# Kernel tuning notes

Hardware: AMD Instinct MI355X
Metric: run time of the kernel (lower is better)

## Reference

```python
import jax, jax.numpy as jnp
import numpy as np

B, NS, H = 131072, 64, 32
# e3nn path normalization (irrep_normalization='component', path_normalization='element')
PW1_0 = float((NS * NS + 25.0) ** -0.5)            # paths into hidden 0e: sqrt(1/(NS^2 + 5*5))
PW1_2 = float((5.0 / (10.0 * NS + 25.0)) ** 0.5)   # paths into hidden 2e: sqrt(5/(NS*5 + 5*NS + 25))
PW2_2 = float((5.0 / (3.0 * H * H)) ** 0.5)        # paths into output 2e: sqrt(5/(3*H^2))
INV_S5 = float(5.0 ** -0.5)                        # w3j(0,2,2) = delta/sqrt(5); w3j(2,2,0) = delta/sqrt(5)

def _wigner3j_222():
    # Real l=2 basis as orthonormal symmetric traceless 3x3 matrices (tr(Ma Mb)=delta).
    # C_abc = tr(sym(Ma Mb) Mc), fully symmetric invariant 3-tensor, Frobenius-normalized to 1
    # (the real Wigner 3j for (2,2,2), up to basis orientation convention).
    s2, s6 = np.sqrt(2.0), np.sqrt(6.0)
    M = np.zeros((5, 3, 3))
    M[0] = np.array([[0., 1, 0], [1, 0, 0], [0, 0, 0]]) / s2   # xy
    M[1] = np.array([[0., 0, 0], [0, 0, 1], [0, 1, 0]]) / s2   # yz
    M[2] = np.diag([-1., -1, 2]) / s6                           # 2z^2-x^2-y^2
    M[3] = np.array([[0., 0, 1], [0, 0, 0], [1, 0, 0]]) / s2   # xz
    M[4] = np.diag([1., -1, 0]) / s2                            # x^2-y^2
    C = np.einsum('aij,bjk,cki->abc', M, M, M)
    C = 0.5 * (C + C.transpose(1, 0, 2))
    return C / np.linalg.norm(C)

C222 = jnp.asarray(_wigner3j_222(), dtype=jnp.float32)

def setup_inputs() -> dict:
    key = jax.random.key(0)
    ks = jax.random.split(key, 14)
    f = jnp.float32
    return {
        'scalars': jax.random.normal(ks[0], (B, NS), f),
        'kernel_t2_sum': jax.random.normal(ks[1], (B, 5), f),
        'mc_t2': jax.random.normal(ks[2], (B, 5), f),
        'coulomb_t2': jax.random.normal(ks[3], (B, 5), f),
        'bs_t2': jax.random.normal(ks[4], (B, 5), f),
        'mopac_coulomb_t2': jax.random.normal(ks[5], (B, 5), f),
        # tp1 weights (e3nn internal weights ~ N(0,1)), one (mul1,mul2,mul_out) block per path
        'w1_sss': jax.random.normal(ks[6], (NS, NS, H), f),   # 0e x 0e -> 0e
        'w1_stt': jax.random.normal(ks[7], (NS, 5, H), f),    # 0e x 2e -> 2e
        'w1_tst': jax.random.normal(ks[8], (5, NS, H), f),    # 2e x 0e -> 2e
        'w1_tts': jax.random.normal(ks[9], (5, 5, H), f),     # 2e x 2e -> 0e
        'w1_ttt': jax.random.normal(ks[10], (5, 5, H), f),    # 2e x 2e -> 2e
        # tp2 weights
        'w2_stt': jax.random.normal(ks[11], (H, H, 1), f),
        'w2_tst': jax.random.normal(ks[12], (H, H, 1), f),
        'w2_ttt': jax.random.normal(ks[13], (H, H, 1), f),
    }

def _forward(scalars, kernel_t2_sum, mc_t2, coulomb_t2, bs_t2, mopac_coulomb_t2,
             w1_sss, w1_stt, w1_tst, w1_tts, w1_ttt, w2_stt, w2_tst, w2_ttt):
    s = scalars                                                        # (B, NS) : NS x 0e
    t = jnp.stack([kernel_t2_sum, mc_t2, coulomb_t2, bs_t2,
                   mopac_coulomb_t2], axis=1)
    # tp1: x (x) x -> hidden (H x 0e + H x 2e)
    h_s = PW1_0 * (jnp.einsum('uvw,bu,bv->bw', w1_sss, s, s)
                   + INV_S5 * jnp.einsum('uvw,bui,bvi->bw', w1_tts, t, t))          # (B, H)
    h_t = PW1_2 * (INV_S5 * jnp.einsum('uvw,bu,bvk->bwk', w1_stt, s, t)
                   + INV_S5 * jnp.einsum('uvw,buk,bv->bwk', w1_tst, t, s)
                   + jnp.einsum('uvw,ijk,bui,bvj->bwk', w1_ttt, C222, t, t))        # (B, H, 5)
    out = PW2_2 * (INV_S5 * jnp.einsum('uvw,bu,bvk->bwk', w2_stt, h_s, h_t)
                   + INV_S5 * jnp.einsum('uvw,buk,bv->bwk', w2_tst, h_t, h_s)
                   + jnp.einsum('uvw,ijk,bui,bvj->bwk', w2_ttt, C222, h_t, h_t))    # (B, 1, 5)
    return out[:, 0, :]                                                             # (B, 5)

def reference(scalars, kernel_t2_sum, mc_t2, coulomb_t2, bs_t2, mopac_coulomb_t2,
              w1_sss, w1_stt, w1_tst, w1_tts, w1_ttt, w2_stt, w2_tst, w2_ttt):
    return _forward(scalars, kernel_t2_sum, mc_t2, coulomb_t2, bs_t2, mopac_coulomb_t2,
                    w1_sss, w1_stt, w1_tst, w1_tts, w1_ttt, w2_stt, w2_tst, w2_ttt)
```

## Files before the change

### kernel.cpp

```cpp
#include <hip/hip_runtime.h>
#include <math.h>
#include <stdint.h>


#define CW1 0.23904572186687872f
#define CW2 0.20701966780270626f
#define CW3 0.11952286093343936f

typedef float f32x4 __attribute__((ext_vector_type(4)));
typedef short bf16x8 __attribute__((ext_vector_type(8)));
typedef uint32_t u32x4 __attribute__((ext_vector_type(4)));

__device__ __forceinline__ uint32_t f2bf(float f) {
  uint32_t x = __float_as_uint(f);
  return (x + 0x7fffu + ((x >> 16) & 1u)) >> 16;
}
__device__ __forceinline__ uint32_t packbf(float lo, float hi) {
  return f2bf(lo) | (f2bf(hi) << 16);
}
__device__ __forceinline__ float bflo(uint32_t d) { return __uint_as_float(d << 16); }
__device__ __forceinline__ float bfhi(uint32_t d) { return __uint_as_float(d & 0xffff0000u); }

#define MF16(a, b, c) __builtin_amdgcn_mfma_f32_16x16x32_bf16((a), (b), (c), 0, 0, 0)

__device__ __align__(16) uint32_t g_bsss16[64 * 2 * 2 * 64 * 4];
__device__ __align__(16) uint32_t g_bst16[5 * 2 * 2 * 64 * 4];
__device__ __align__(16) uint32_t g_btts16[2 * 64 * 4];
__device__ __align__(16) uint32_t g_bttt16[2 * 64 * 4];
__device__ __align__(16) uint32_t g_bg2_16[2 * 64 * 4];
__device__ __align__(16) uint32_t g_bgt16[2 * 64 * 4];

__device__ const int c_pu[16] = {0,0,0,0,0,1,1,1,1,2,2,2,3,3,4,0};
__device__ const int c_pv[16] = {0,1,2,3,4,1,2,3,4,2,3,4,3,4,4,0};

__global__ void ech_prep(const float* __restrict__ w1_sss, const float* __restrict__ w1_stt,
                         const float* __restrict__ w1_tst, const float* __restrict__ w1_tts,
                         const float* __restrict__ w1_ttt, const float* __restrict__ w2_stt,
                         const float* __restrict__ w2_tst, const float* __restrict__ w2_ttt) {
  const float PW1_0 = (float)(1.0 / sqrt(4121.0));
  const float PW1_2 = (float)sqrt(5.0 / 665.0);
  const float PW2_2 = (float)sqrt(5.0 / 3072.0);
  const float IS5   = (float)sqrt(0.2);

  int idx = blockIdx.x * 256 + threadIdx.x;

  if (idx < 65536) {
    int d = idx & 3, l = (idx >> 2) & 63, c = (idx >> 8) & 1, n = (idx >> 9) & 1, v = idx >> 10;
    int gg = l >> 4, w = n * 16 + (l & 15);
    int u0 = 32 * c + 8 * gg + 2 * d, u1 = u0 + 1;
    float lo = 0.f, hi = 0.f;
    if (u0 < v)       lo = w1_sss[(u0 * 64 + v) * 32 + w] + w1_sss[(v * 64 + u0) * 32 + w];
    else if (u0 == v) lo = w1_sss[(u0 * 64 + v) * 32 + w];
    if (u1 < v)       hi = w1_sss[(u1 * 64 + v) * 32 + w] + w1_sss[(v * 64 + u1) * 32 + w];
    else if (u1 == v) hi = w1_sss[(u1 * 64 + v) * 32 + w];
    g_bsss16[idx] = packbf(PW1_0 * lo, PW1_0 * hi);
    return;
  }
  idx -= 65536;
  if (idx < 5120) {
    int d = idx & 3, l = (idx >> 2) & 63, c = (idx >> 8) & 1, n = (idx >> 9) & 1, ct = idx >> 10;
    int gg = l >> 4, w = n * 16 + (l & 15);
    float sc = PW1_2 * IS5;
    int u0 = 32 * c + 8 * gg + 2 * d, u1 = u0 + 1;
    g_bst16[idx] = packbf(sc * (w1_stt[(u0 * 5 + ct) * 32 + w] + w1_tst[(ct * 64 + u0) * 32 + w]),
                          sc * (w1_stt[(u1 * 5 + ct) * 32 + w] + w1_tst[(ct * 64 + u1) * 32 + w]));
    return;
  }
  idx -= 5120;
  if (idx < 512) {
    int d = idx & 3, l = (idx >> 2) & 63, n = idx >> 8;
    int gg = l >> 4, w = n * 16 + (l & 15);
    float sc = PW1_0 * IS5;
    float val[2];
#pragma unroll
    for (int q = 0; q < 2; ++q) {
      int p = 8 * gg + 2 * d + q;
      float x = 0.f;
      if (p < 15) {
        int u = c_pu[p], v = c_pv[p];
        x = w1_tts[(u * 5 + v) * 32 + w];
        if (u < v) x += w1_tts[(v * 5 + u) * 32 + w];
        x *= sc;
      }
      val[q] = x;
    }
    g_btts16[idx] = packbf(val[0], val[1]);
    return;
  }
  idx -= 512;
  if (idx < 512) {
    int d = idx & 3, l = (idx >> 2) & 63, n = idx >> 8;
    int gg = l >> 4, w = n * 16 + (l & 15);
    float val[2];
#pragma unroll
    for (int q = 0; q < 2; ++q) {
      int p = 8 * gg + 2 * d + q;
      float x = 0.f;
      if (p < 15) {
        int u = c_pu[p], v = c_pv[p];
        x = w1_ttt[(u * 5 + v) * 32 + w];
        if (u < v) x += w1_ttt[(v * 5 + u) * 32 + w];
        x *= PW1_2;
      }
      val[q] = x;
    }
    g_bttt16[idx] = packbf(val[0], val[1]);
    return;
  }
  idx -= 512;
  if (idx < 512) {
    int d = idx & 3, l = (idx >> 2) & 63, n = idx >> 8;
    int gg = l >> 4, v = n * 16 + (l & 15);
    float sc = PW2_2 * IS5;
    int u0 = 8 * gg + 2 * d, u1 = u0 + 1;
    g_bg2_16[idx] = packbf(sc * (w2_stt[u0 * 32 + v] + w2_tst[v * 32 + u0]),
                           sc * (w2_stt[u1 * 32 + v] + w2_tst[v * 32 + u1]));
    return;
  }
  idx -= 512;
  if (idx < 512) {
    int d = idx & 3, l = (idx >> 2) & 63, n = idx >> 8;
    int gg = l >> 4, v = n * 16 + (l & 15);
    int u0 = 8 * gg + 2 * d, u1 = u0 + 1;
    g_bgt16[idx] = packbf(PW2_2 * w2_ttt[u0 * 32 + v], PW2_2 * w2_ttt[u1 * 32 + v]);
    return;
  }
}

#define S_STRIDE 33
#define OFF_SF 2112
#define SF_STRIDE 65
#define OFF_T 6272
#define ED_STRIDE 49
#define PLANE(i) ((i) * 1088)
#define LDS_DW 7872

__global__ __launch_bounds__(256, 2)
void ech_fused(const float* __restrict__ scalars,
               const float* __restrict__ tk, const float* __restrict__ tm,
               const float* __restrict__ tc, const float* __restrict__ tb,
               const float* __restrict__ tmc,
               float* __restrict__ out) {
  __shared__ uint32_t lds[LDS_DW];

  const int tid = threadIdx.x;
  const int rows64 = blockIdx.x * 64;
  const int wave = tid >> 6, lane = tid & 63;
  const int g = lane >> 4, col16 = lane & 15;
  const int wrow = wave * 16;
  const f32x4 zero4 = {0.f, 0.f, 0.f, 0.f};

#pragma unroll
  for (int it = 0; it < 8; ++it) {
    int di = it * 256 + tid;
    int row = di >> 5, j = di & 31;
    float f0 = scalars[(rows64 + row) * 64 + 2 * j];
    float f1 = scalars[(rows64 + row) * 64 + 2 * j + 1];
    lds[row * S_STRIDE + j] = packbf(f0, f1);
    lds[OFF_SF + row * SF_STRIDE + 2 * j]     = __float_as_uint(f0);
    lds[OFF_SF + row * SF_STRIDE + 2 * j + 1] = __float_as_uint(f1);
  }
#pragma unroll
  for (int v = 0; v < 5; ++v) {
    const float* p = (v == 0 ? tk : v == 1 ? tm : v == 2 ? tc : v == 3 ? tb : tmc);
#pragma unroll
    for (int it = 0; it < 2; ++it) {
      int i = it * 256 + tid;
      if (i < 320)
        lds[OFF_T + (i / 5) * 25 + v * 5 + (i % 5)] = __float_as_uint(p[rows64 * 5 + i]);
    }
  }
  __syncthreads();

  bf16x8 afr_hi[2];
#pragma unroll
  for (int c = 0; c < 2; ++c) {
    int base = (wrow + col16) * S_STRIDE + 16 * c + 4 * g;
    u32x4 th;
    th.x = lds[base + 0]; th.y = lds[base + 1];
    th.z = lds[base + 2]; th.w = lds[base + 3];
    afr_hi[c] = __builtin_bit_cast(bf16x8, th);
  }

  f32x4 hsA = zero4, hsB = zero4;
  const bf16x8* gb = (const bf16x8*)g_bsss16;
#pragma unroll 2
  for (int vd = 0; vd < 16; ++vd) {
    int v0 = 2 * vd, v1 = v0 + 1;
    bf16x8 b00 = gb[(v0 * 4 + 0) * 64 + lane];
    bf16x8 b01 = gb[(v0 * 4 + 2) * 64 + lane];
    bf16x8 b10 = gb[(v1 * 4 + 0) * 64 + lane];
    bf16x8 b11 = gb[(v1 * 4 + 2) * 64 + lane];
    f32x4 Z00 = MF16(afr_hi[0], b00, zero4);
    f32x4 Z01 = MF16(afr_hi[0], b01, zero4);
    f32x4 Z10 = MF16(afr_hi[0], b10, zero4);
    f32x4 Z11 = MF16(afr_hi[0], b11, zero4);
#pragma unroll
    for (int r = 0; r < 4; ++r) {
      int row = wrow + 4 * g + r;
      float s0 = __uint_as_float(lds[OFF_SF + row * SF_STRIDE + v0]);
      float s1 = __uint_as_float(lds[OFF_SF + row * SF_STRIDE + v1]);
      hsA[r] = fmaf(s0, Z00[r], hsA[r]); hsA[r] = fmaf(s1, Z10[r], hsA[r]);
      hsB[r] = fmaf(s0, Z01[r], hsB[r]); hsB[r] = fmaf(s1, Z11[r], hsB[r]);
    }
  }
#pragma unroll 2
  for (int vd = 16; vd < 32; ++vd) {
    int v0 = 2 * vd, v1 = v0 + 1;
    f32x4 Z00 = zero4, Z01 = zero4, Z10 = zero4, Z11 = zero4;
#pragma unroll
    for (int c = 0; c < 2; ++c) {
      bf16x8 b00 = gb[(v0 * 4 + 0 + c) * 64 + lane];
      bf16x8 b01 = gb[(v0 * 4 + 2 + c) * 64 + lane];
      bf16x8 b10 = gb[(v1 * 4 + 0 + c) * 64 + lane];
      bf16x8 b11 = gb[(v1 * 4 + 2 + c) * 64 + lane];
      Z00 = MF16(afr_hi[c], b00, Z00);
      Z01 = MF16(afr_hi[c], b01, Z01);
      Z10 = MF16(afr_hi[c], b10, Z10);
      Z11 = MF16(afr_hi[c], b11, Z11);
    }
#pragma unroll
    for (int r = 0; r < 4; ++r) {
      int row = wrow + 4 * g + r;
      float s0 = __uint_as_float(lds[OFF_SF + row * SF_STRIDE + v0]);
      float s1 = __uint_as_float(lds[OFF_SF + row * SF_STRIDE + v1]);
      hsA[r] = fmaf(s0, Z00[r], hsA[r]); hsA[r] = fmaf(s1, Z10[r], hsA[r]);
      hsB[r] = fmaf(s0, Z01[r], hsB[r]); hsB[r] = fmaf(s1, Z11[r], hsB[r]);
    }
  }

  f32x4 ht[5][2];
#pragma unroll
  for (int k = 0; k < 5; ++k) { ht[k][0] = zero4; ht[k][1] = zero4; }
  {
    const bf16x8* gs = (const bf16x8*)g_bst16;
#pragma unroll
    for (int ct = 0; ct < 5; ++ct) {
      f32x4 a0 = zero4, a1 = zero4;
#pragma unroll
      for (int c = 0; c < 2; ++c) {
        bf16x8 b0 = gs[(ct * 4 + 0 + c) * 64 + lane];
        bf16x8 b1 = gs[(ct * 4 + 2 + c) * 64 + lane];
        a0 = MF16(afr_hi[c], b0, a0);
        a1 = MF16(afr_hi[c], b1, a1);
      }
#pragma unroll
      for (int r = 0; r < 4; ++r) {
        int row = wrow + 4 * g + r;
        int tbi = OFF_T + row * 25 + ct * 5;
        float t0 = __uint_as_float(lds[tbi + 0]);
        float t1 = __uint_as_float(lds[tbi + 1]);
        float t2 = __uint_as_float(lds[tbi + 2]);
        float t3 = __uint_as_float(lds[tbi + 3]);
        float t4 = __uint_as_float(lds[tbi + 4]);
        ht[0][0][r] = fmaf(a0[r], t0, ht[0][0][r]); ht[0][1][r] = fmaf(a1[r], t0, ht[0][1][r]);
        ht[1][0][r] = fmaf(a0[r], t1, ht[1][0][r]); ht[1][1][r] = fmaf(a1[r], t1, ht[1][1][r]);
        ht[2][0][r] = fmaf(a0[r], t2, ht[2][0][r]); ht[2][1][r] = fmaf(a1[r], t2, ht[2][1][r]);
        ht[3][0][r] = fmaf(a0[r], t3, ht[3][0][r]); ht[3][1][r] = fmaf(a1[r], t3, ht[3][1][r]);
        ht[4][0][r] = fmaf(a0[r], t4, ht[4][0][r]); ht[4][1][r] = fmaf(a1[r], t4, ht[4][1][r]);
      }
    }
  }
  __syncthreads();

  {
    int row = tid >> 2, part = tid & 3;
    int tbase = OFF_T + row * 25;
    float P[4][6];
#pragma unroll
    for (int q = 0; q < 4; ++q) {
      int p = part * 4 + q;
      int U = c_pu[p], V = c_pv[p];
      float a0 = __uint_as_float(lds[tbase + U * 5 + 0]);
      float a1 = __uint_as_float(lds[tbase + U * 5 + 1]);
      float a2 = __uint_as_float(lds[tbase + U * 5 + 2]);
      float a3 = __uint_as_float(lds[tbase + U * 5 + 3]);
      float a4 = __uint_as_float(lds[tbase + U * 5 + 4]);
      float b0 = __uint_as_float(lds[tbase + V * 5 + 0]);
      float b1 = __uint_as_float(lds[tbase + V * 5 + 1]);
      float b2 = __uint_as_float(lds[tbase + V * 5 + 2]);
      float b3 = __uint_as_float(lds[tbase + V * 5 + 3]);
      float b4 = __uint_as_float(lds[tbase + V * 5 + 4]);
      float d0 = a0 * b0, d1 = a1 * b1, d2 = a2 * b2, d3 = a3 * b3, d4 = a4 * b4;
      float s01 = a0 * b1 + a1 * b0;
      float s02 = a0 * b2 + a2 * b0;
      float s03 = a0 * b3 + a3 * b0;
      float s12 = a1 * b2 + a2 * b1;
      float s13 = a1 * b3 + a3 * b1;
      float s14 = a1 * b4 + a4 * b1;
      float s23 = a2 * b3 + a3 * b2;
      float s24 = a2 * b4 + a4 * b2;
      float s34 = a3 * b4 + a4 * b3;
      P[q][0] = -CW1 * s02 + CW2 * s13;
      P[q][1] = CW2 * s03 + CW3 * s12 - CW2 * s14;
      P[q][2] = -CW1 * d0 + CW3 * d1 + CW1 * d2 + CW3 * d3 - CW1 * d4;
      P[q][3] = CW2 * s01 + CW3 * s23 + CW2 * s34;
      P[q][4] = -CW2 * d1 - CW1 * s24 + CW2 * d3;
      P[q][5] = d0 + d1 + d2 + d3 + d4;
      if (p == 15) {
#pragma unroll
        for (int c6 = 0; c6 < 6; ++c6) P[q][c6] = 0.f;
      }
    }
    int rb = row * ED_STRIDE + part * 2;
#pragma unroll
    for (int comp = 0; comp < 6; ++comp) {
      lds[rb + comp * 8 + 0] = packbf(P[0][comp], P[1][comp]);
      lds[rb + comp * 8 + 1] = packbf(P[2][comp], P[3][comp]);
    }
  }
  __syncthreads();

  {
    int arow = wrow + col16;
    int gl = g & 1;
    bool gok = (g < 2);
    {
      int b5 = arow * ED_STRIDE + 40 + 4 * gl;
      u32x4 tmp;
      tmp.x = gok ? lds[b5 + 0] : 0u;
      tmp.y = gok ? lds[b5 + 1] : 0u;
      tmp.z = gok ? lds[b5 + 2] : 0u;
      tmp.w = gok ? lds[b5 + 3] : 0u;
      bf16x8 dfr = __builtin_bit_cast(bf16x8, tmp);
      hsA = MF16(dfr, ((const bf16x8*)g_btts16)[lane], hsA);
      hsB = MF16(dfr, ((const bf16x8*)g_btts16)[64 + lane], hsB);
    }
    bf16x8 btt0 = ((const bf16x8*)g_bttt16)[lane];
    bf16x8 btt1 = ((const bf16x8*)g_bttt16)[64 + lane];
#pragma unroll
    for (int k = 0; k < 5; ++k) {
      int bk = arow * ED_STRIDE + k * 8 + 4 * gl;
      u32x4 tmp;
      tmp.x = gok ? lds[bk + 0] : 0u;
      tmp.y = gok ? lds[bk + 1] : 0u;
      tmp.z = gok ? lds[bk + 2] : 0u;
      tmp.w = gok ? lds[bk + 3] : 0u;
      bf16x8 efr = __builtin_bit_cast(bf16x8, tmp);
      ht[k][0] = MF16(efr, btt0, ht[k][0]);
      ht[k][1] = MF16(efr, btt1, ht[k][1]);
    }
  }
  __syncthreads();

#pragma unroll
  for (int r = 0; r < 4; ++r) {
    int row = wrow + 4 * g + r;
    int dwb = row * 17 + (col16 >> 1);
    float pA = __shfl_xor(hsA[r], 1, 64);
    float pB = __shfl_xor(hsB[r], 1, 64);
    if (!(col16 & 1)) {
      lds[PLANE(0) + dwb]     = packbf(hsA[r], pA);
      lds[PLANE(0) + dwb + 8] = packbf(hsB[r], pB);
    }
#pragma unroll
    for (int k = 0; k < 5; ++k) {
      float qA = __shfl_xor(ht[k][0][r], 1, 64);
      float qB = __shfl_xor(ht[k][1][r], 1, 64);
      if (!(col16 & 1)) {
        lds[PLANE(1 + k) + dwb]     = packbf(ht[k][0][r], qA);
        lds[PLANE(1 + k) + dwb + 8] = packbf(ht[k][1][r], qB);
      }
    }
  }

  f32x4 g2n[2];
  {
    int prow = wrow + col16;
    int b = PLANE(0) + prow * 17 + 4 * g;
    u32x4 tmp;
    tmp.x = lds[b]; tmp.y = lds[b + 1]; tmp.z = lds[b + 2]; tmp.w = lds[b + 3];
    bf16x8 af = __builtin_bit_cast(bf16x8, tmp);
    g2n[0] = MF16(af, ((const bf16x8*)g_bg2_16)[lane], zero4);
    g2n[1] = MF16(af, ((const bf16x8*)g_bg2_16)[64 + lane], zero4);
  }
  f32x4 gt[5][2];
#pragma unroll
  for (int i = 0; i < 5; ++i) {
    int prow = wrow + col16;
    int b = PLANE(1 + i) + prow * 17 + 4 * g;
    u32x4 tmp;
    tmp.x = lds[b]; tmp.y = lds[b + 1]; tmp.z = lds[b + 2]; tmp.w = lds[b + 3];
    bf16x8 af = __builtin_bit_cast(bf16x8, tmp);
    gt[i][0] = MF16(af, ((const bf16x8*)g_bgt16)[lane], zero4);
    gt[i][1] = MF16(af, ((const bf16x8*)g_bgt16)[64 + lane], zero4);
  }

#define REDSTORE(K)                                                        \
  {                                                                        \
    _Pragma("unroll") for (int m = 1; m <= 8; m <<= 1)                     \
        _Pragma("unroll") for (int r = 0; r < 4; ++r)                      \
            tot[r] += __shfl_xor(tot[r], m, 64);                           \
    if (col16 == (K)) {                                                    \
      _Pragma("unroll") for (int r = 0; r < 4; ++r)                        \
          out[(size_t)(rows64 + wrow + 4 * g + r) * 5 + (K)] = tot[r];     \
    }                                                                      \
  }

  {
    float tot[4];
#pragma unroll
    for (int r = 0; r < 4; ++r) {
      float s = 0.f;
#pragma unroll
      for (int n = 0; n < 2; ++n) {
        float ok = g2n[n][r] * ht[0][n][r];
        ok = fmaf(-CW1, gt[0][n][r] * ht[2][n][r] + gt[2][n][r] * ht[0][n][r], ok);
        ok = fmaf( CW2, gt[1][n][r] * ht[3][n][r] + gt[3][n][r] * ht[1][n][r], ok);
        s += ok;
      }
      tot[r] = s;
    }
    REDSTORE(0)
  }
  {
    float tot[4];
#pragma unroll
    for (int r = 0; r < 4; ++r) {
      float s = 0.f;
#pragma unroll
      for (int n = 0; n < 2; ++n) {
        float ok = g2n[n][r] * ht[1][n][r];
        ok = fmaf( CW2, gt[0][n][r] * ht[3][n][r] + gt[3][n][r] * ht[0][n][r], ok);
        ok = fmaf( CW3, gt[1][n][r] * ht[2][n][r] + gt[2][n][r] * ht[1][n][r], ok);
        ok = fmaf(-CW2, gt[1][n][r] * ht[4][n][r] + gt[4][n][r] * ht[1][n][r], ok);
        s += ok;
      }
      tot[r] = s;
    }
    REDSTORE(1)
  }
  {
    float tot[4];
#pragma unroll
    for (int r = 0; r < 4; ++r) {
      float s = 0.f;
#pragma unroll
      for (int n = 0; n < 2; ++n) {
        float ok = g2n[n][r] * ht[2][n][r];
        ok = fmaf(-CW1, gt[0][n][r] * ht[0][n][r], ok);
        ok = fmaf( CW3, gt[1][n][r] * ht[1][n][r], ok);
        ok = fmaf( CW1, gt[2][n][r] * ht[2][n][r], ok);
        ok = fmaf( CW3, gt[3][n][r] * ht[3][n][r], ok);
        ok = fmaf(-CW1, gt[4][n][r] * ht[4][n][r], ok);
        s += ok;
      }
      tot[r] = s;
    }
    REDSTORE(2)
  }
  {
    float tot[4];
#pragma unroll
    for (int r = 0; r < 4; ++r) {
      float s = 0.f;
#pragma unroll
      for (int n = 0; n < 2; ++n) {
        float ok = g2n[n][r] * ht[3][n][r];
        ok = fmaf( CW2, gt[0][n][r] * ht[1][n][r] + gt[1][n][r] * ht[0][n][r], ok);
        ok = fmaf( CW3, gt[2][n][r] * ht[3][n][r] + gt[3][n][r] * ht[2][n][r], ok);
        ok = fmaf( CW2, gt[3][n][r] * ht[4][n][r] + gt[4][n][r] * ht[3][n][r], ok);
        s += ok;
      }
      tot[r] = s;
    }
    REDSTORE(3)
  }
  {
    float tot[4];
#pragma unroll
    for (int r = 0; r < 4; ++r) {
      float s = 0.f;
#pragma unroll
      for (int n = 0; n < 2; ++n) {
        float ok = g2n[n][r] * ht[4][n][r];
        ok = fmaf(-CW2, gt[1][n][r] * ht[1][n][r], ok);
        ok = fmaf(-CW1, gt[2][n][r] * ht[4][n][r] + gt[4][n][r] * ht[2][n][r], ok);
        ok = fmaf( CW2, gt[3][n][r] * ht[3][n][r], ok);
        s += ok;
      }
      tot[r] = s;
    }
    REDSTORE(4)
  }
}

extern "C" void kernel_launch(void* const* d_in, const int* in_sizes, int n_in,
                              void* d_out, int out_size, void* d_ws, size_t ws_size,
                              hipStream_t stream) {
  (void)n_in; (void)out_size; (void)d_ws; (void)ws_size;
  const float* scalars = (const float*)d_in[0];
  const float* tk  = (const float*)d_in[1];
  const float* tm  = (const float*)d_in[2];
  const float* tc  = (const float*)d_in[3];
  const float* tb  = (const float*)d_in[4];
  const float* tmc = (const float*)d_in[5];

  ech_prep<<<284, 256, 0, stream>>>((const float*)d_in[6], (const float*)d_in[7],
                                    (const float*)d_in[8], (const float*)d_in[9],
                                    (const float*)d_in[10], (const float*)d_in[11],
                                    (const float*)d_in[12], (const float*)d_in[13]);

  const int B = in_sizes[0] / 64;
  ech_fused<<<B / 64, 256, 0, stream>>>(scalars, tk, tm, tc, tb, tmc, (float*)d_out);
}
```

Measured before the change: 95.80 us.

## Split fused kernel into hidden-scalar kernel and remaining tensor-path kernel

Splits the single fused kernel into two launches. The first computes the scalar hidden features h_s with a smaller LDS footprint and higher launch-bounds occupancy, then writes them to a workspace buffer. The second re-reads scalars and the tensor inputs, loads h_s from the workspace, and does the rest. This aims to relieve register and LDS pressure in the heavy dense stage. The cost is an extra launch, a second read of scalars, and a round trip of the B×32 intermediate through global memory. Both branches of the workspace-size check run the same code, so an undersized workspace is not handled.

```diff
diff --git a/kernel.cpp b/kernel.cpp
--- a/kernel.cpp
+++ b/kernel.cpp
@@ -18,8 +18,6 @@
 __device__ __forceinline__ uint32_t packbf(float lo, float hi) {
   return f2bf(lo) | (f2bf(hi) << 16);
 }
-__device__ __forceinline__ float bflo(uint32_t d) { return __uint_as_float(d << 16); }
-__device__ __forceinline__ float bfhi(uint32_t d) { return __uint_as_float(d & 0xffff0000u); }
 
 #define MF16(a, b, c) __builtin_amdgcn_mfma_f32_16x16x32_bf16((a), (b), (c), 0, 0, 0)
 
@@ -127,22 +125,14 @@
   }
 }
 
-#define S_STRIDE 33
-#define OFF_SF 2112
-#define SF_STRIDE 65
-#define OFF_T 6272
-#define ED_STRIDE 49
-#define PLANE(i) ((i) * 1088)
-#define LDS_DW 7872
-
-__global__ __launch_bounds__(256, 2)
-void ech_fused(const float* __restrict__ scalars,
-               const float* __restrict__ tk, const float* __restrict__ tm,
-               const float* __restrict__ tc, const float* __restrict__ tb,
-               const float* __restrict__ tmc,
-               float* __restrict__ out) {
-  __shared__ uint32_t lds[LDS_DW];
-
+#define K1_SST 33
+#define K1_SF 2112
+#define K1_SFST 65
+#define K1_LDS 6272
+
+__global__ __launch_bounds__(256, 4)
+void ech_hs(const float* __restrict__ scalars, float* __restrict__ hsws) {
+  __shared__ uint32_t lds[K1_LDS];
   const int tid = threadIdx.x;
   const int rows64 = blockIdx.x * 64;
   const int wave = tid >> 6, lane = tid & 63;
@@ -156,26 +146,16 @@
     int row = di >> 5, j = di & 31;
     float f0 = scalars[(rows64 + row) * 64 + 2 * j];
     float f1 = scalars[(rows64 + row) * 64 + 2 * j + 1];
-    lds[row * S_STRIDE + j] = packbf(f0, f1);
-    lds[OFF_SF + row * SF_STRIDE + 2 * j]     = __float_as_uint(f0);
-    lds[OFF_SF + row * SF_STRIDE + 2 * j + 1] = __float_as_uint(f1);
-  }
-#pragma unroll
-  for (int v = 0; v < 5; ++v) {
-    const float* p = (v == 0 ? tk : v == 1 ? tm : v == 2 ? tc : v == 3 ? tb : tmc);
-#pragma unroll
-    for (int it = 0; it < 2; ++it) {
-      int i = it * 256 + tid;
-      if (i < 320)
-        lds[OFF_T + (i / 5) * 25 + v * 5 + (i % 5)] = __float_as_uint(p[rows64 * 5 + i]);
-    }
+    lds[row * K1_SST + j] = packbf(f0, f1);
+    lds[K1_SF + row * K1_SFST + 2 * j]     = __float_as_uint(f0);
+    lds[K1_SF + row * K1_SFST + 2 * j + 1] = __float_as_uint(f1);
   }
   __syncthreads();
 
   bf16x8 afr_hi[2];
 #pragma unroll
   for (int c = 0; c < 2; ++c) {
-    int base = (wrow + col16) * S_STRIDE + 16 * c + 4 * g;
+    int base = (wrow + col16) * K1_SST + 16 * c + 4 * g;
     u32x4 th;
     th.x = lds[base + 0]; th.y = lds[base + 1];
     th.z = lds[base + 2]; th.w = lds[base + 3];
@@ -198,8 +178,8 @@
 #pragma unroll
     for (int r = 0; r < 4; ++r) {
       int row = wrow + 4 * g + r;
-      float s0 = __uint_as_float(lds[OFF_SF + row * SF_STRIDE + v0]);
-      float s1 = __uint_as_float(lds[OFF_SF + row * SF_STRIDE + v1]);
+      float s0 = __uint_as_float(lds[K1_SF + row * K1_SFST + v0]);
+      float s1 = __uint_as_float(lds[K1_SF + row * K1_SFST + v1]);
       hsA[r] = fmaf(s0, Z00[r], hsA[r]); hsA[r] = fmaf(s1, Z10[r], hsA[r]);
       hsB[r] = fmaf(s0, Z01[r], hsB[r]); hsB[r] = fmaf(s1, Z11[r], hsB[r]);
     }
@@ -222,11 +202,79 @@
 #pragma unroll
     for (int r = 0; r < 4; ++r) {
       int row = wrow + 4 * g + r;
-      float s0 = __uint_as_float(lds[OFF_SF + row * SF_STRIDE + v0]);
-      float s1 = __uint_as_float(lds[OFF_SF + row * SF_STRIDE + v1]);
+      float s0 = __uint_as_float(lds[K1_SF + row * K1_SFST + v0]);
+      float s1 = __uint_as_float(lds[K1_SF + row * K1_SFST + v1]);
       hsA[r] = fmaf(s0, Z00[r], hsA[r]); hsA[r] = fmaf(s1, Z10[r], hsA[r]);
       hsB[r] = fmaf(s0, Z01[r], hsB[r]); hsB[r] = fmaf(s1, Z11[r], hsB[r]);
     }
+  }
+
+#pragma unroll
+  for (int r = 0; r < 4; ++r) {
+    size_t row = (size_t)(rows64 + wrow + 4 * g + r);
+    hsws[row * 32 + col16]      = hsA[r];
+    hsws[row * 32 + 16 + col16] = hsB[r];
+  }
+}
+
+#define K2_SST 33
+#define K2_T 2112
+#define K2_ED 3712
+#define ED_STRIDE 49
+#define PLANE(i) ((i) * 1088)
+#define K2_LDS 6848
+
+__global__ __launch_bounds__(256, 2)
+void ech_rest(const float* __restrict__ scalars,
+              const float* __restrict__ tk, const float* __restrict__ tm,
+              const float* __restrict__ tc, const float* __restrict__ tb,
+              const float* __restrict__ tmc,
+              const float* __restrict__ hsws,
+              float* __restrict__ out) {
+  __shared__ uint32_t lds[K2_LDS];
+  const int tid = threadIdx.x;
+  const int rows64 = blockIdx.x * 64;
+  const int wave = tid >> 6, lane = tid & 63;
+  const int g = lane >> 4, col16 = lane & 15;
+  const int wrow = wave * 16;
+  const f32x4 zero4 = {0.f, 0.f, 0.f, 0.f};
+
+#pragma unroll
+  for (int it = 0; it < 8; ++it) {
+    int di = it * 256 + tid;
+    int row = di >> 5, j = di & 31;
+    float f0 = scalars[(rows64 + row) * 64 + 2 * j];
+    float f1 = scalars[(rows64 + row) * 64 + 2 * j + 1];
+    lds[row * K2_SST + j] = packbf(f0, f1);
+  }
+#pragma unroll
+  for (int v = 0; v < 5; ++v) {
+    const float* p = (v == 0 ? tk : v == 1 ? tm : v == 2 ? tc : v == 3 ? tb : tmc);
+#pragma unroll
+    for (int it = 0; it < 2; ++it) {
+      int i = it * 256 + tid;
+      if (i < 320)
+        lds[K2_T + (i / 5) * 25 + v * 5 + (i % 5)] = __float_as_uint(p[rows64 * 5 + i]);
+    }
+  }
+  __syncthreads();
+
+  f32x4 hsA, hsB;
+#pragma unroll
+  for (int r = 0; r < 4; ++r) {
+    size_t row = (size_t)(rows64 + wrow + 4 * g + r);
+    hsA[r] = hsws[row * 32 + col16];
+    hsB[r] = hsws[row * 32 + 16 + col16];
+  }
+
+  bf16x8 afr_hi[2];
+#pragma unroll
+  for (int c = 0; c < 2; ++c) {
+    int base = (wrow + col16) * K2_SST + 16 * c + 4 * g;
+    u32x4 th;
+    th.x = lds[base + 0]; th.y = lds[base + 1];
+    th.z = lds[base + 2]; th.w = lds[base + 3];
+    afr_hi[c] = __builtin_bit_cast(bf16x8, th);
   }
 
   f32x4 ht[5][2];
@@ -247,7 +295,7 @@
 #pragma unroll
       for (int r = 0; r < 4; ++r) {
         int row = wrow + 4 * g + r;
-        int tbi = OFF_T + row * 25 + ct * 5;
+        int tbi = K2_T + row * 25 + ct * 5;
         float t0 = __uint_as_float(lds[tbi + 0]);
         float t1 = __uint_as_float(lds[tbi + 1]);
         float t2 = __uint_as_float(lds[tbi + 2]);
@@ -261,11 +309,10 @@
       }
     }
   }
-  __syncthreads();
 
   {
     int row = tid >> 2, part = tid & 3;
-    int tbase = OFF_T + row * 25;
+    int tbase = K2_T + row * 25;
     float P[4][6];
 #pragma unroll
     for (int q = 0; q < 4; ++q) {
@@ -302,7 +349,7 @@
         for (int c6 = 0; c6 < 6; ++c6) P[q][c6] = 0.f;
       }
     }
-    int rb = row * ED_STRIDE + part * 2;
+    int rb = K2_ED + row * ED_STRIDE + part * 2;
 #pragma unroll
     for (int comp = 0; comp < 6; ++comp) {
       lds[rb + comp * 8 + 0] = packbf(P[0][comp], P[1][comp]);
@@ -316,7 +363,7 @@
     int gl = g & 1;
     bool gok = (g < 2);
     {
-      int b5 = arow * ED_STRIDE + 40 + 4 * gl;
+      int b5 = K2_ED + arow * ED_STRIDE + 40 + 4 * gl;
       u32x4 tmp;
       tmp.x = gok ? lds[b5 + 0] : 0u;
       tmp.y = gok ? lds[b5 + 1] : 0u;
@@ -330,7 +377,7 @@
     bf16x8 btt1 = ((const bf16x8*)g_bttt16)[64 + lane];
 #pragma unroll
     for (int k = 0; k < 5; ++k) {
-      int bk = arow * ED_STRIDE + k * 8 + 4 * gl;
+      int bk = K2_ED + arow * ED_STRIDE + k * 8 + 4 * gl;
       u32x4 tmp;
       tmp.x = gok ? lds[bk + 0] : 0u;
       tmp.y = gok ? lds[bk + 1] : 0u;
@@ -488,7 +535,7 @@
 extern "C" void kernel_launch(void* const* d_in, const int* in_sizes, int n_in,
                               void* d_out, int out_size, void* d_ws, size_t ws_size,
                               hipStream_t stream) {
-  (void)n_in; (void)out_size; (void)d_ws; (void)ws_size;
+  (void)n_in; (void)out_size;
   const float* scalars = (const float*)d_in[0];
   const float* tk  = (const float*)d_in[1];
   const float* tm  = (const float*)d_in[2];
@@ -502,5 +549,16 @@
                                     (const float*)d_in[12], (const float*)d_in[13]);
 
   const int B = in_sizes[0] / 64;
-  ech_fused<<<B / 64, 256, 0, stream>>>(scalars, tk, tm, tc, tb, tmc, (float*)d_out);
+  const size_t need = (size_t)B * 32 * sizeof(float);
+  if (ws_size >= need) {
+    float* hsws = (float*)d_ws;
+    ech_hs<<<B / 64, 256, 0, stream>>>(scalars, hsws);
+    ech_rest<<<B / 64, 256, 0, stream>>>(scalars, tk, tm, tc, tb, tmc, hsws,
+                                         (float*)d_out);
+  } else {
+    float* hsws = (float*)d_ws;
+    ech_hs<<<B / 64, 256, 0, stream>>>(scalars, hsws);
+    ech_rest<<<B / 64, 256, 0, stream>>>(scalars, tk, tm, tc, tb, tmc, hsws,
+                                         (float*)d_out);
+  }
 }
```

Measured after the change: 109.5 us. 14.3% more time.
